# Optimization experiments

Hardware: AMD Instinct MI355X
Metric: run time of the kernel (lower is better)

## Reference

```python
import jax, jax.numpy as jnp
import numpy as np

# NCHW 3x3 conv, padding=1. BatchNorm (inference affine) is folded into conv weight/bias,
# which is mathematically identical to Conv->BN(eval) in the original.
def conv3(x, w, b, stride):
    y = jax.lax.conv_general_dilated(x, w, (stride, stride), [(1, 1), (1, 1)],
                                     dimension_numbers=('NCHW', 'OIHW', 'NCHW'))
    return y + b[None, :, None, None]

def lin1(x, w, b):  # 1x1 conv as channel matmul; w: [out, in]
    return jnp.einsum('oc,bchw->bohw', w, x) + b[None, :, None, None]

def setup_inputs():
    key = jax.random.key(0)
    ks = list(jax.random.split(key, 32))
    C, M = 32, 32  # cv_hypo_num, mid_dim (kq_dim == mid_dim since mid_dim <= 128)
    B, H, W = 1, 256, 512
    w3 = lambda k, o, i: jax.random.normal(k, (o, i, 3, 3), jnp.float32) * 0.05
    w1 = lambda k, o, i: jax.random.normal(k, (o, i), jnp.float32) * 0.05
    bv = lambda k, o: jax.random.normal(k, (o,), jnp.float32) * 0.01
    inp = {
        'mono_pseudo_cost': jax.random.normal(ks[0], (B, C, H, W), jnp.float32),
        'cost_volume': jax.random.normal(ks[1], (B, C, H, W), jnp.float32),
        # mono_expand / multi_expand: two stride-2 conv(+folded BN)+ReLU blocks each
        'me_w1': w3(ks[2], M, C), 'me_b1': bv(ks[3], M),
        'me_w2': w3(ks[4], M, C), 'me_b2': bv(ks[5], M),
        'xe_w1': w3(ks[6], M, C), 'xe_b1': bv(ks[7], M),
        'xe_w2': w3(ks[8], M, C), 'xe_b2': bv(ks[9], M),
        # 1x1 q/k/v projections for both branches
        'mq_w': w1(ks[10], M, M), 'mq_b': bv(ks[11], M),
        'mk_w': w1(ks[12], M, M), 'mk_b': bv(ks[13], M),
        'mv_w': w1(ks[14], M, M), 'mv_b': bv(ks[15], M),
        'xq_w': w1(ks[16], M, M), 'xq_b': bv(ks[17], M),
        'xk_w': w1(ks[18], M, M), 'xk_b': bv(ks[19], M),
        'xv_w': w1(ks[20], M, M), 'xv_b': bv(ks[21], M),
        # residual branches
        'mr_w1': w3(ks[22], M, C), 'mr_b1': bv(ks[23], M),
        'mr_w2': w3(ks[24], M, C), 'mr_b2': bv(ks[25], M),
        'xr_w': w1(ks[26], M, C), 'xr_b': bv(ks[27], M),
        'gamma': jnp.full((1,), 0.5, jnp.float32),  # nonzero so attention path is live
    }
    return inp

def reference(mono_pseudo_cost, cost_volume,
              me_w1, me_b1, me_w2, me_b2,
              xe_w1, xe_b1, xe_w2, xe_b2,
              mq_w, mq_b, mk_w, mk_b, mv_w, mv_b,
              xq_w, xq_b, xk_w, xk_b, xv_w, xv_b,
              mr_w1, mr_b1, mr_w2, mr_b2,
              xr_w, xr_b, gamma):
    relu = jax.nn.relu
    init_h, init_w = cost_volume.shape[2], cost_volume.shape[3]
    M = me_w1.shape[0]
    # feature extractors (stride-2 x2): [B,32,256,512] -> [B,32,64,128]
    mono_feat = relu(conv3(relu(conv3(mono_pseudo_cost, me_w1, me_b1, 2)), me_w2, me_b2, 2))
    multi_feat = relu(conv3(relu(conv3(cost_volume, xe_w1, xe_b1, 2)), xe_w2, xe_b2, 2))
    b, c, h, w = multi_feat.shape
    hw = h * w
    # q/k/v as [B, C, hw]
    mono_q = lin1(mono_feat, mq_w, mq_b).reshape(b, -1, hw)
    mono_k = lin1(mono_feat, mk_w, mk_b).reshape(b, -1, hw)
    mono_v = lin1(mono_feat, mv_w, mv_b).reshape(b, -1, hw)
    multi_q = lin1(multi_feat, xq_w, xq_b).reshape(b, -1, hw)
    multi_k = lin1(multi_feat, xk_w, xk_b).reshape(b, -1, hw)
    multi_v = lin1(multi_feat, xv_w, xv_b).reshape(b, -1, hw)
    # full [B, hw, hw] attention, no 1/sqrt(d) scaling (as in original)
    mono_atten = jax.nn.softmax(jnp.einsum('bci,bcj->bij', mono_q, mono_k), axis=-1)
    multi_atten = jax.nn.softmax(jnp.einsum('bci,bcj->bij', multi_q, multi_k), axis=-1)
    # cross application: mono values weighted by multi attention and vice versa
    mono_out = jnp.einsum('bcj,bij->bci', mono_v, multi_atten).reshape(b, M, h, w)
    multi_out = jnp.einsum('bcj,bij->bci', multi_v, mono_atten).reshape(b, M, h, w)
    fused = jnp.concatenate([multi_out, mono_out], axis=1)
    # nearest-neighbor upsample back to input size (integer factor 4)
    fused = jnp.repeat(jnp.repeat(fused, init_h // h, axis=2), init_w // w, axis=3)
    # residual branches
    mono_residual = relu(conv3(relu(conv3(mono_pseudo_cost, mr_w1, mr_b1, 1)), mr_w2, mr_b2, 1))
    multi_residual = relu(lin1(cost_volume, xr_w, xr_b))
    fused = jnp.concatenate([mono_residual, multi_residual], axis=1) + gamma * fused
    return fused
```

## Files before the change

### kernel.cpp

```cpp
#include <hip/hip_runtime.h>


using bf16x8 = __attribute__((ext_vector_type(8))) short;
using f32x4  = __attribute__((ext_vector_type(4))) float;
using f32x16 = __attribute__((ext_vector_type(16))) float;
typedef unsigned short u16;
typedef unsigned int   u32;

__device__ __forceinline__ u16 f2bf(float f) {
  u32 u = __builtin_bit_cast(u32, f);
  u = (u + 0x7fffu + ((u >> 16) & 1u)) >> 16;
  return (u16)u;
}
__device__ __forceinline__ float bf2f(u16 v) {
  u32 u = ((u32)v) << 16;
  return __builtin_bit_cast(float, u);
}
__device__ __forceinline__ float bfLO(u32 u) { return __builtin_bit_cast(float, u << 16); }
__device__ __forceinline__ float bfHI(u32 u) { return __builtin_bit_cast(float, u & 0xffff0000u); }
__device__ __forceinline__ u32 pktr(float lo, float hi) {
  return __builtin_amdgcn_perm(__builtin_bit_cast(u32, hi),
                               __builtin_bit_cast(u32, lo), 0x07060302u);
}
__device__ __forceinline__ f32x4 mfma16(bf16x8 a, bf16x8 b, f32x4 c) {
  return __builtin_amdgcn_mfma_f32_16x16x32_bf16(a, b, c, 0, 0, 0);
}
__device__ __forceinline__ f32x16 mfma32(bf16x8 a, bf16x8 b, f32x16 c) {
  return __builtin_amdgcn_mfma_f32_32x32x16_bf16(a, b, c, 0, 0, 0);
}
__device__ __forceinline__ f32x16 zero16() {
  f32x16 z = {0,0,0,0,0,0,0,0,0,0,0,0,0,0,0,0};
  return z;
}
__device__ __forceinline__ void store4bf(u16* dst, f32x4 v) {
  u32 lo = (u32)f2bf(v[0]) | ((u32)f2bf(v[1]) << 16);
  u32 hi = (u32)f2bf(v[2]) | ((u32)f2bf(v[3]) << 16);
  *(uint2*)dst = make_uint2(lo, hi);
}
__device__ __forceinline__ float sum16(const float* e) {
  float s0 = e[0] + e[1], s1 = e[2] + e[3], s2 = e[4] + e[5], s3 = e[6] + e[7];
  float s4 = e[8] + e[9], s5 = e[10] + e[11], s6 = e[12] + e[13], s7 = e[14] + e[15];
  float a = s0 + s1, b = s2 + s3, c = s4 + s5, d = s6 + s7;
  return (a + b) + (c + d);
}

struct WPtrs { const float* p[13]; };

__global__ void k_pre(WPtrs wp, u16* __restrict__ wConv, u16* __restrict__ w1x1,
                      const float* __restrict__ mono, const float* __restrict__ cv,
                      u16* __restrict__ monoT, u16* __restrict__ cvT,
                      u16* __restrict__ m1T, u16* __restrict__ x1T, u16* __restrict__ r1T) {
  int bx = blockIdx.x, t = threadIdx.x;
  if (bx < 13) {
    if (bx < 6) {
      const float* s = wp.p[bx];
      u16* d = wConv + bx * 9216;
      for (int i = t; i < 9216; i += 256) {
        int tap = i >> 10, co = (i >> 5) & 31, ci = i & 31;
        d[i] = f2bf(s[co * 288 + ci * 9 + tap]);
      }
    } else {
      const float* s = wp.p[bx];
      u16* d = w1x1 + (bx - 6) * 1024;
      for (int i = t; i < 1024; i += 256) d[i] = f2bf(s[i]);
    }
    return;
  }
  if (bx < 138) {
    int zb = bx - 13;
    int buf = zb % 5, blk = zb / 5;
    u16* b; int Hp, Wp;
    switch (buf) {
      case 0: b = monoT; Hp = 258; Wp = 514; break;
      case 1: b = cvT;   Hp = 258; Wp = 514; break;
      case 2: b = m1T;   Hp = 130; Wp = 258; break;
      case 3: b = x1T;   Hp = 130; Wp = 258; break;
      default: b = r1T;  Hp = 258; Wp = 514; break;
    }
    int id = blk * 256 + t;
    int cell = id >> 2, c8 = (id & 3) << 3;
    if (cell >= 2 * (Hp + Wp)) return;
    int r, c;
    if (cell < Wp)              { r = 0;                 c = cell; }
    else if (cell < 2 * Wp)     { r = Hp - 1;            c = cell - Wp; }
    else if (cell < 2 * Wp + Hp){ r = cell - 2 * Wp;     c = 0; }
    else                        { r = cell - 2 * Wp - Hp; c = Wp - 1; }
    bf16x8 z = {0, 0, 0, 0, 0, 0, 0, 0};
    *(bf16x8*)&b[(r * Wp + c) * 32 + c8] = z;
    return;
  }
  int idx = bx - 138;
  int xb = idx & 7, y = (idx >> 3) & 255, z = idx >> 11;
  const float* src = z ? cv : mono;
  u16* dst = z ? cvT : monoT;
  int x0 = xb << 6;
  __shared__ u16 tile[64][40];
  int ci = t >> 3, kx = (t & 7) << 3;
  const float* sp = src + ci * 131072 + y * 512 + x0 + kx;
  float4 a = *(const float4*)sp;
  float4 bb = *(const float4*)(sp + 4);
  tile[kx + 0][ci] = f2bf(a.x); tile[kx + 1][ci] = f2bf(a.y);
  tile[kx + 2][ci] = f2bf(a.z); tile[kx + 3][ci] = f2bf(a.w);
  tile[kx + 4][ci] = f2bf(bb.x); tile[kx + 5][ci] = f2bf(bb.y);
  tile[kx + 6][ci] = f2bf(bb.z); tile[kx + 7][ci] = f2bf(bb.w);
  __syncthreads();
  int x = t >> 2, c8 = (t & 3) << 3;
  bf16x8 v = *(bf16x8*)&tile[x][c8];
  *(bf16x8*)(dst + ((y + 1) * 514 + (x0 + x + 1)) * 32 + c8) = v;
}

__device__ __forceinline__ void conv3x3_body(int bxl, int tid,
    const u16* __restrict__ inT, int Wp, const u16* __restrict__ w9,
    const float* __restrict__ bias, u16* __restrict__ out, int outPitch,
    int outOff, int Ho, int tprShift, int stride) {
  int wid = (bxl * 256 + tid) >> 6;
  int lane = tid & 63, ln = lane & 15, q = lane >> 4;
  int y = wid >> tprShift;
  int x0 = (wid & ((1 << tprShift) - 1)) << 4;
  if (y >= Ho) return;
  f32x4 acc0 = *(const f32x4*)(bias + q * 4);
  f32x4 acc1 = *(const f32x4*)(bias + 16 + q * 4);
  const u16* ib = inT + (stride * y * Wp + stride * (x0 + ln)) * 32 + q * 8;
  const u16* wb = w9 + ln * 32 + q * 8;
#pragma unroll
  for (int dy = 0; dy < 3; ++dy)
#pragma unroll
    for (int dx = 0; dx < 3; ++dx) {
      int tap = dy * 3 + dx;
      bf16x8 bf = *(const bf16x8*)(ib + (dy * Wp + dx) * 32);
      acc0 = mfma16(*(const bf16x8*)(wb + tap * 1024), bf, acc0);
      acc1 = mfma16(*(const bf16x8*)(wb + tap * 1024 + 512), bf, acc1);
    }
#pragma unroll
  for (int r = 0; r < 4; ++r) { acc0[r] = fmaxf(acc0[r], 0.f); acc1[r] = fmaxf(acc1[r], 0.f); }
  u16* ob = out + (outOff + y * outPitch + x0 + ln) * 32;
  store4bf(ob + q * 4, acc0);
  store4bf(ob + 16 + q * 4, acc1);
}

__global__ void k_convs(const u16* __restrict__ monoT, const u16* __restrict__ cvT,
                        const u16* __restrict__ wConv,
                        const float* me_b1, const float* xe_b1, const float* mr_b1,
                        u16* __restrict__ m1T, u16* __restrict__ x1T, u16* __restrict__ r1T) {
  int bx = blockIdx.x;
  if (bx < 512)
    conv3x3_body(bx, threadIdx.x, monoT, 514, wConv + 0 * 9216, me_b1, m1T, 258, 259, 128, 4, 2);
  else if (bx < 1024)
    conv3x3_body(bx - 512, threadIdx.x, cvT, 514, wConv + 2 * 9216, xe_b1, x1T, 258, 259, 128, 4, 2);
  else
    conv3x3_body(bx - 1024, threadIdx.x, monoT, 514, wConv + 4 * 9216, mr_b1, r1T, 514, 515, 256, 5, 1);
}

__global__ void k_featproj(const u16* __restrict__ m1T, const u16* __restrict__ x1T,
                           const u16* __restrict__ wConv, const u16* __restrict__ w1x1,
                           const float* me_b2, const float* xe_b2,
                           const float* mq_b, const float* mk_b, const float* mv_b,
                           const float* xq_b, const float* xk_b, const float* xv_b,
                           u16* Qm, u16* Km, u16* Vm, u16* Qx, u16* Kx, u16* Vx) {
  int bx = blockIdx.x, br = blockIdx.y;
  const u16* inT = br ? x1T : m1T;
  const u16* w9 = wConv + (br ? 3 : 1) * 9216;
  const float* bias2 = br ? xe_b2 : me_b2;
  __shared__ u16 fs[64][40];
  int tid = threadIdx.x, wave = tid >> 6, lane = tid & 63, ln = lane & 15, q = lane >> 4;
  int fy = bx >> 1, x0 = (bx & 1) * 64 + wave * 16;
  {
    f32x4 acc0 = *(const f32x4*)(bias2 + q * 4);
    f32x4 acc1 = *(const f32x4*)(bias2 + 16 + q * 4);
    const u16* ib = inT + (2 * fy * 258 + 2 * (x0 + ln)) * 32 + q * 8;
    const u16* wb = w9 + ln * 32 + q * 8;
#pragma unroll
    for (int dy = 0; dy < 3; ++dy)
#pragma unroll
      for (int dx = 0; dx < 3; ++dx) {
        int tap = dy * 3 + dx;
        bf16x8 bf = *(const bf16x8*)(ib + (dy * 258 + dx) * 32);
        acc0 = mfma16(*(const bf16x8*)(wb + tap * 1024), bf, acc0);
        acc1 = mfma16(*(const bf16x8*)(wb + tap * 1024 + 512), bf, acc1);
      }
#pragma unroll
    for (int r = 0; r < 4; ++r) { acc0[r] = fmaxf(acc0[r], 0.f); acc1[r] = fmaxf(acc1[r], 0.f); }
    int row = wave * 16 + ln;
    store4bf(&fs[row][q * 4], acc0);
    store4bf(&fs[row][16 + q * 4], acc1);
  }
  __syncthreads();
  int p = fy * 128 + x0 + ln;
  bf16x8 bf = *(const bf16x8*)&fs[wave * 16 + ln][q * 8];
#pragma unroll
  for (int wh = 0; wh < 3; ++wh) {
    int which = br * 3 + wh;
    const float* bias; u16* dst; float scale = 1.f; int cmode = 0;
    switch (which) {
      case 0: bias = mq_b; dst = Qm; scale = 1.4426950408889634f; break;
      case 1: bias = mk_b; dst = Km; break;
      case 2: bias = mv_b; dst = Vm; cmode = 1; break;
      case 3: bias = xq_b; dst = Qx; scale = 1.4426950408889634f; break;
      case 4: bias = xk_b; dst = Kx; break;
      default: bias = xv_b; dst = Vx; cmode = 1; break;
    }
    const u16* w = w1x1 + which * 1024;
    bf16x8 a0 = *(const bf16x8*)(w + ln * 32 + q * 8);
    bf16x8 a1 = *(const bf16x8*)(w + (16 + ln) * 32 + q * 8);
    f32x4 acc0 = *(const f32x4*)(bias + q * 4);
    f32x4 acc1 = *(const f32x4*)(bias + 16 + q * 4);
    acc0 = mfma16(a0, bf, acc0);
    acc1 = mfma16(a1, bf, acc1);
#pragma unroll
    for (int r = 0; r < 4; ++r) { acc0[r] *= scale; acc1[r] *= scale; }
    if (!cmode) {
      store4bf(dst + p * 32 + q * 4, acc0);
      store4bf(dst + p * 32 + 16 + q * 4, acc1);
    } else {
      int jl = p & 63, jb = p & ~63;
      int pj = jb + (jl >> 5) * 32 + ((jl >> 4) & 1) * 16 + ((jl >> 2) & 1) * 8
             + ((jl >> 3) & 1) * 4 + (jl & 3);
#pragma unroll
      for (int r = 0; r < 4; ++r) {
        dst[(q * 4 + r) * 8192 + pj] = f2bf(acc0[r]);
        dst[(16 + q * 4 + r) * 8192 + pj] = f2bf(acc1[r]);
      }
    }
  }
}

__global__ void __launch_bounds__(256, 4) k_attention(
    const u16* __restrict__ Qm, const u16* __restrict__ Km, const u16* __restrict__ Vm,
    const u16* __restrict__ Qx, const u16* __restrict__ Kx, const u16* __restrict__ Vx,
    u16* __restrict__ Opart, float* __restrict__ lpart) {
  const u16 *Qp, *Kp, *Vp;
  int att = blockIdx.z;
  if (att == 0) { Qp = Qm; Kp = Km; Vp = Vx; }
  else          { Qp = Qx; Kp = Kx; Vp = Vm; }
  int sp = blockIdx.y;
  int j0 = sp << 10;

  __shared__ u16 Kl[2][64][40];
  __shared__ u16 Vl[2][32][72];

  int t = threadIdx.x, wave = t >> 6, lane = t & 63, ln = lane & 31, h = lane >> 5;
  int iw = blockIdx.x * 128 + wave * 32;

  bf16x8 qf0 = *(const bf16x8*)(Qp + (iw + ln) * 32 + h * 8);
  bf16x8 qf1 = *(const bf16x8*)(Qp + (iw + ln) * 32 + 16 + h * 8);

  int krow = t >> 2, kcol = (t & 3) << 3;
  int vrow = t >> 3, vcol = (t & 7) << 3;
  const u16* Kg = Kp + j0 * 32;
  const u16* Vg = Vp + j0;

  bf16x8 kn = *(const bf16x8*)(Kg + t * 8);
  bf16x8 vn = *(const bf16x8*)(Vg + vrow * 8192 + vcol);
  *(bf16x8*)&Kl[0][krow][kcol] = kn;
  *(bf16x8*)&Vl[0][vrow][vcol] = vn;

  f32x16 O = zero16();
  float lsum = 0.f;

  for (int jt = 0; jt < 16; ++jt) {
    __syncthreads();
    bool have = (jt + 1) < 16;
    if (have) {
      kn = *(const bf16x8*)(Kg + (jt + 1) * 2048 + t * 8);
      vn = *(const bf16x8*)(Vg + vrow * 8192 + (jt + 1) * 64 + vcol);
    }
    int cur = jt & 1;
#pragma unroll
    for (int hh = 0; hh < 2; ++hh) {
      f32x16 s = mfma32(*(const bf16x8*)&Kl[cur][hh * 32 + ln][h * 8], qf0, zero16());
      s = mfma32(*(const bf16x8*)&Kl[cur][hh * 32 + ln][16 + h * 8], qf1, s);
      float e[16];
#pragma unroll
      for (int r = 0; r < 16; ++r) e[r] = __builtin_amdgcn_exp2f(s[r]);
      lsum += sum16(e);
      union PF { bf16x8 v; u32 w[4]; } pf0, pf1;
#pragma unroll
      for (int p = 0; p < 4; ++p) {
        pf0.w[p] = pktr(e[2 * p], e[2 * p + 1]);
        pf1.w[p] = pktr(e[8 + 2 * p], e[8 + 2 * p + 1]);
      }
      bf16x8 vf0 = *(const bf16x8*)&Vl[cur][ln][(2 * hh) * 16 + h * 8];
      bf16x8 vf1 = *(const bf16x8*)&Vl[cur][ln][(2 * hh + 1) * 16 + h * 8];
      O = mfma32(pf0.v, vf0, O);
      O = mfma32(pf1.v, vf1, O);
    }
    if (have) {
      *(bf16x8*)&Kl[1 - cur][krow][kcol] = kn;
      *(bf16x8*)&Vl[1 - cur][vrow][vcol] = vn;
    }
  }
  u16* ob = Opart + (size_t)(att * 8 + sp) * 262144;
  float* lb = lpart + (att * 8 + sp) * 8192;
#pragma unroll
  for (int r = 0; r < 16; ++r) {
    int ig = iw + (r & 3) + 8 * (r >> 2) + 4 * h;
    ob[ig * 32 + ln] = f2bf(O[r]);
  }
  float lo = __shfl(lsum, lane ^ 32, 64);
  float lt = lsum + lo;
  if (lane < 32) lb[iw + lane] = lt;
}

__device__ __forceinline__ void att_reduce(const u16* __restrict__ Opart,
                                           const float* __restrict__ lpart,
                                           int a, int apix, int q, float g,
                                           f32x4& vA, f32x4& vB) {
  f32x4 sA = {0, 0, 0, 0}, sB = {0, 0, 0, 0};
  float l = 0.f;
#pragma unroll
  for (int sp = 0; sp < 8; ++sp) {
    const u16* op = Opart + (size_t)(a * 8 + sp) * 262144 + apix * 32;
    uint2 w0 = *(const uint2*)(op + q * 4);
    uint2 w1 = *(const uint2*)(op + 16 + q * 4);
    sA[0] += bfLO(w0.x); sA[1] += bfHI(w0.x); sA[2] += bfLO(w0.y); sA[3] += bfHI(w0.y);
    sB[0] += bfLO(w1.x); sB[1] += bfHI(w1.x); sB[2] += bfLO(w1.y); sB[3] += bfHI(w1.y);
    l += lpart[(a * 8 + sp) * 8192 + apix];
  }
  float gl = g / l;
#pragma unroll
  for (int r = 0; r < 4; ++r) { vA[r] = sA[r] * gl; vB[r] = sB[r] * gl; }
}

__global__ void k_final(const u16* __restrict__ r1T, const u16* __restrict__ cvT,
                        const u16* __restrict__ wConv, const u16* __restrict__ w1x1,
                        const float* mr_b2, const float* xr_b,
                        const u16* __restrict__ Opart, const float* __restrict__ lpart,
                        const float* __restrict__ gamma, float* __restrict__ dout) {
  int bx = blockIdx.x, tid = threadIdx.x;
  int lane = tid & 63, ln = lane & 15, q = lane >> 4;
  float g = gamma[0];
  if (bx < 2048) {
    const u16* w9 = wConv + 5 * 9216;
    int wid = (bx * 256 + tid) >> 6;
    int y = wid >> 5, x0 = (wid & 31) << 4;
    f32x4 acc0 = *(const f32x4*)(mr_b2 + q * 4);
    f32x4 acc1 = *(const f32x4*)(mr_b2 + 16 + q * 4);
    const u16* ib = r1T + (y * 514 + x0 + ln) * 32 + q * 8;
    const u16* wb = w9 + ln * 32 + q * 8;
#pragma unroll
    for (int dy = 0; dy < 3; ++dy)
#pragma unroll
      for (int dx = 0; dx < 3; ++dx) {
        int tap = dy * 3 + dx;
        bf16x8 bf = *(const bf16x8*)(ib + (dy * 514 + dx) * 32);
        acc0 = mfma16(*(const bf16x8*)(wb + tap * 1024), bf, acc0);
        acc1 = mfma16(*(const bf16x8*)(wb + tap * 1024 + 512), bf, acc1);
      }
    int xg = x0 + ln;
    int apix = (y >> 2) * 128 + (xg >> 2);
    f32x4 vA, vB;
    att_reduce(Opart, lpart, 0, apix, q, g, vA, vB);
    float* ob = dout + y * 512 + xg;
#pragma unroll
    for (int r = 0; r < 4; ++r) {
      int co0 = q * 4 + r, co1 = 16 + q * 4 + r;
      ob[co0 * 131072] = fmaxf(acc0[r], 0.f) + vA[r];
      ob[co1 * 131072] = fmaxf(acc1[r], 0.f) + vB[r];
    }
  } else {
    const u16* w = w1x1 + 6 * 1024;
    int wid = ((bx - 2048) * 256 + tid) >> 6;
    int p0 = wid << 4;
    int y = p0 >> 9, x0 = p0 & 511;
    bf16x8 bf = *(const bf16x8*)(cvT + ((y + 1) * 514 + x0 + ln + 1) * 32 + q * 8);
    f32x4 acc0 = *(const f32x4*)(xr_b + q * 4);
    f32x4 acc1 = *(const f32x4*)(xr_b + 16 + q * 4);
    acc0 = mfma16(*(const bf16x8*)(w + ln * 32 + q * 8), bf, acc0);
    acc1 = mfma16(*(const bf16x8*)(w + (16 + ln) * 32 + q * 8), bf, acc1);
    int xg = x0 + ln;
    int apix = (y >> 2) * 128 + (xg >> 2);
    f32x4 vA, vB;
    att_reduce(Opart, lpart, 1, apix, q, g, vA, vB);
    float* ob = dout + 32 * 131072 + p0 + ln;
#pragma unroll
    for (int r = 0; r < 4; ++r) {
      int co0 = q * 4 + r, co1 = 16 + q * 4 + r;
      ob[co0 * 131072] = fmaxf(acc0[r], 0.f) + vA[r];
      ob[co1 * 131072] = fmaxf(acc1[r], 0.f) + vB[r];
    }
  }
}

extern "C" void kernel_launch(void* const* d_in, const int* in_sizes, int n_in,
                              void* d_out, int out_size, void* d_ws, size_t ws_size,
                              hipStream_t stream) {
  const float* mono  = (const float*)d_in[0];
  const float* cv    = (const float*)d_in[1];
  const float* me_b1 = (const float*)d_in[3];
  const float* me_b2 = (const float*)d_in[5];
  const float* xe_b1 = (const float*)d_in[7];
  const float* xe_b2 = (const float*)d_in[9];
  const float* mq_b  = (const float*)d_in[11];
  const float* mk_b  = (const float*)d_in[13];
  const float* mv_b  = (const float*)d_in[15];
  const float* xq_b  = (const float*)d_in[17];
  const float* xk_b  = (const float*)d_in[19];
  const float* xv_b  = (const float*)d_in[21];
  const float* mr_b1 = (const float*)d_in[23];
  const float* mr_b2 = (const float*)d_in[25];
  const float* xr_b  = (const float*)d_in[27];
  const float* gamma = (const float*)d_in[28];
  float* dout = (float*)d_out;

  char* ws = (char*)d_ws;
  u16* wConv = (u16*)(ws + 0);
  u16* w1x1  = (u16*)(ws + 110592);
  u16* monoT = (u16*)(ws + 124928);
  u16* Opart = (u16*)(ws + 124928);
  u16* cvT   = (u16*)(ws + 8612096);
  u16* m1T   = (u16*)(ws + 17099264);
  u16* x1T   = (u16*)(ws + 19245824);
  u16* r1T   = (u16*)(ws + 21392384);
  u16* Qm    = (u16*)(ws + 30928128);
  u16* Km    = (u16*)(ws + 31452416);
  u16* Vm    = (u16*)(ws + 31976704);
  u16* Qx    = (u16*)(ws + 32500992);
  u16* Kx    = (u16*)(ws + 33025280);
  u16* Vx    = (u16*)(ws + 33549568);
  float* lpart = (float*)(ws + 36171008);

  WPtrs wp;
  wp.p[0] = (const float*)d_in[2];
  wp.p[1] = (const float*)d_in[4];
  wp.p[2] = (const float*)d_in[6];
  wp.p[3] = (const float*)d_in[8];
  wp.p[4] = (const float*)d_in[22];
  wp.p[5] = (const float*)d_in[24];
  wp.p[6] = (const float*)d_in[10];
  wp.p[7] = (const float*)d_in[12];
  wp.p[8] = (const float*)d_in[14];
  wp.p[9] = (const float*)d_in[16];
  wp.p[10] = (const float*)d_in[18];
  wp.p[11] = (const float*)d_in[20];
  wp.p[12] = (const float*)d_in[26];

  k_pre<<<4234, 256, 0, stream>>>(wp, wConv, w1x1, mono, cv, monoT, cvT, m1T, x1T, r1T);
  k_convs<<<3072, 256, 0, stream>>>(monoT, cvT, wConv, me_b1, xe_b1, mr_b1, m1T, x1T, r1T);
  k_featproj<<<dim3(128, 2), 256, 0, stream>>>(m1T, x1T, wConv, w1x1, me_b2, xe_b2,
                                               mq_b, mk_b, mv_b, xq_b, xk_b, xv_b,
                                               Qm, Km, Vm, Qx, Kx, Vx);
  k_attention<<<dim3(64, 8, 2), 256, 0, stream>>>(Qm, Km, Vm, Qx, Kx, Vx, Opart, lpart);
  k_final<<<4096, 256, 0, stream>>>(r1T, cvT, wConv, w1x1, mr_b2, xr_b, Opart, lpart, gamma, dout);
}
```

Before: 214.6 us.

## Fuse residual full-res conv into attention launch and double attention K/V tile

```diff
diff --git a/kernel.cpp b/kernel.cpp
--- a/kernel.cpp
+++ b/kernel.cpp
@@ -140,15 +140,13 @@
 
 __global__ void k_convs(const u16* __restrict__ monoT, const u16* __restrict__ cvT,
                         const u16* __restrict__ wConv,
-                        const float* me_b1, const float* xe_b1, const float* mr_b1,
-                        u16* __restrict__ m1T, u16* __restrict__ x1T, u16* __restrict__ r1T) {
+                        const float* me_b1, const float* xe_b1,
+                        u16* __restrict__ m1T, u16* __restrict__ x1T) {
   int bx = blockIdx.x;
   if (bx < 512)
     conv3x3_body(bx, threadIdx.x, monoT, 514, wConv + 0 * 9216, me_b1, m1T, 258, 259, 128, 4, 2);
-  else if (bx < 1024)
+  else
     conv3x3_body(bx - 512, threadIdx.x, cvT, 514, wConv + 2 * 9216, xe_b1, x1T, 258, 259, 128, 4, 2);
-  else
-    conv3x3_body(bx - 1024, threadIdx.x, monoT, 514, wConv + 4 * 9216, mr_b1, r1T, 514, 515, 256, 5, 1);
 }
 
 __global__ void k_featproj(const u16* __restrict__ m1T, const u16* __restrict__ x1T,
@@ -224,51 +222,62 @@
   }
 }
 
-__global__ void __launch_bounds__(256, 4) k_attention(
+__global__ void __launch_bounds__(256, 4) k_attnconv(
     const u16* __restrict__ Qm, const u16* __restrict__ Km, const u16* __restrict__ Vm,
     const u16* __restrict__ Qx, const u16* __restrict__ Kx, const u16* __restrict__ Vx,
-    u16* __restrict__ Opart, float* __restrict__ lpart) {
+    const u16* __restrict__ monoT, const u16* __restrict__ wConv, const float* mr_b1,
+    u16* __restrict__ r1T, u16* __restrict__ Opart, float* __restrict__ lpart) {
+  int vb = blockIdx.x;
+  if (vb >= 1024) {
+    conv3x3_body(vb - 1024, threadIdx.x, monoT, 514, wConv + 4 * 9216, mr_b1,
+                 r1T, 514, 515, 256, 5, 1);
+    return;
+  }
+  int ib = vb & 63, sp = (vb >> 6) & 7, att = vb >> 9;
   const u16 *Qp, *Kp, *Vp;
-  int att = blockIdx.z;
   if (att == 0) { Qp = Qm; Kp = Km; Vp = Vx; }
   else          { Qp = Qx; Kp = Kx; Vp = Vm; }
-  int sp = blockIdx.y;
-  int j0 = sp << 10;
-
-  __shared__ u16 Kl[2][64][40];
-  __shared__ u16 Vl[2][32][72];
+
+  __shared__ u16 Kl[2][128][40];
+  __shared__ u16 Vl[2][32][136];
 
   int t = threadIdx.x, wave = t >> 6, lane = t & 63, ln = lane & 31, h = lane >> 5;
-  int iw = blockIdx.x * 128 + wave * 32;
+  int iw = ib * 128 + wave * 32;
 
   bf16x8 qf0 = *(const bf16x8*)(Qp + (iw + ln) * 32 + h * 8);
   bf16x8 qf1 = *(const bf16x8*)(Qp + (iw + ln) * 32 + 16 + h * 8);
 
-  int krow = t >> 2, kcol = (t & 3) << 3;
-  int vrow = t >> 3, vcol = (t & 7) << 3;
-  const u16* Kg = Kp + j0 * 32;
-  const u16* Vg = Vp + j0;
-
-  bf16x8 kn = *(const bf16x8*)(Kg + t * 8);
-  bf16x8 vn = *(const bf16x8*)(Vg + vrow * 8192 + vcol);
-  *(bf16x8*)&Kl[0][krow][kcol] = kn;
-  *(bf16x8*)&Vl[0][vrow][vcol] = vn;
+  int krow = t >> 1, kcol = (t & 1) << 4;
+  int vrow = t >> 3, vcol = (t & 7) << 4;
+  const u16* Kg = Kp + sp * 32768;
+  const u16* Vg = Vp + sp * 1024;
+
+  bf16x8 kn0 = *(const bf16x8*)(Kg + t * 16);
+  bf16x8 kn1 = *(const bf16x8*)(Kg + t * 16 + 8);
+  bf16x8 vn0 = *(const bf16x8*)(Vg + vrow * 8192 + vcol);
+  bf16x8 vn1 = *(const bf16x8*)(Vg + vrow * 8192 + vcol + 8);
+  *(bf16x8*)&Kl[0][krow][kcol] = kn0;
+  *(bf16x8*)&Kl[0][krow][kcol + 8] = kn1;
+  *(bf16x8*)&Vl[0][vrow][vcol] = vn0;
+  *(bf16x8*)&Vl[0][vrow][vcol + 8] = vn1;
 
   f32x16 O = zero16();
   float lsum = 0.f;
 
-  for (int jt = 0; jt < 16; ++jt) {
+  for (int jt = 0; jt < 8; ++jt) {
     __syncthreads();
-    bool have = (jt + 1) < 16;
+    bool have = (jt + 1) < 8;
     if (have) {
-      kn = *(const bf16x8*)(Kg + (jt + 1) * 2048 + t * 8);
-      vn = *(const bf16x8*)(Vg + vrow * 8192 + (jt + 1) * 64 + vcol);
+      kn0 = *(const bf16x8*)(Kg + (jt + 1) * 4096 + t * 16);
+      kn1 = *(const bf16x8*)(Kg + (jt + 1) * 4096 + t * 16 + 8);
+      vn0 = *(const bf16x8*)(Vg + vrow * 8192 + (jt + 1) * 128 + vcol);
+      vn1 = *(const bf16x8*)(Vg + vrow * 8192 + (jt + 1) * 128 + vcol + 8);
     }
     int cur = jt & 1;
 #pragma unroll
-    for (int hh = 0; hh < 2; ++hh) {
-      f32x16 s = mfma32(*(const bf16x8*)&Kl[cur][hh * 32 + ln][h * 8], qf0, zero16());
-      s = mfma32(*(const bf16x8*)&Kl[cur][hh * 32 + ln][16 + h * 8], qf1, s);
+    for (int g = 0; g < 4; ++g) {
+      f32x16 s = mfma32(*(const bf16x8*)&Kl[cur][g * 32 + ln][h * 8], qf0, zero16());
+      s = mfma32(*(const bf16x8*)&Kl[cur][g * 32 + ln][16 + h * 8], qf1, s);
       float e[16];
 #pragma unroll
       for (int r = 0; r < 16; ++r) e[r] = __builtin_amdgcn_exp2f(s[r]);
@@ -279,14 +288,16 @@
         pf0.w[p] = pktr(e[2 * p], e[2 * p + 1]);
         pf1.w[p] = pktr(e[8 + 2 * p], e[8 + 2 * p + 1]);
       }
-      bf16x8 vf0 = *(const bf16x8*)&Vl[cur][ln][(2 * hh) * 16 + h * 8];
-      bf16x8 vf1 = *(const bf16x8*)&Vl[cur][ln][(2 * hh + 1) * 16 + h * 8];
+      bf16x8 vf0 = *(const bf16x8*)&Vl[cur][ln][g * 32 + h * 8];
+      bf16x8 vf1 = *(const bf16x8*)&Vl[cur][ln][g * 32 + 16 + h * 8];
       O = mfma32(pf0.v, vf0, O);
       O = mfma32(pf1.v, vf1, O);
     }
     if (have) {
-      *(bf16x8*)&Kl[1 - cur][krow][kcol] = kn;
-      *(bf16x8*)&Vl[1 - cur][vrow][vcol] = vn;
+      *(bf16x8*)&Kl[1 - cur][krow][kcol] = kn0;
+      *(bf16x8*)&Kl[1 - cur][krow][kcol + 8] = kn1;
+      *(bf16x8*)&Vl[1 - cur][vrow][vcol] = vn0;
+      *(bf16x8*)&Vl[1 - cur][vrow][vcol + 8] = vn1;
     }
   }
   u16* ob = Opart + (size_t)(att * 8 + sp) * 262144;
@@ -406,7 +417,6 @@
   u16* wConv = (u16*)(ws + 0);
   u16* w1x1  = (u16*)(ws + 110592);
   u16* monoT = (u16*)(ws + 124928);
-  u16* Opart = (u16*)(ws + 124928);
   u16* cvT   = (u16*)(ws + 8612096);
   u16* m1T   = (u16*)(ws + 17099264);
   u16* x1T   = (u16*)(ws + 19245824);
@@ -418,6 +428,7 @@
   u16* Kx    = (u16*)(ws + 33025280);
   u16* Vx    = (u16*)(ws + 33549568);
   float* lpart = (float*)(ws + 36171008);
+  u16* Opart = (u16*)(ws + 37219840);
 
   WPtrs wp;
   wp.p[0] = (const float*)d_in[2];
@@ -435,10 +446,11 @@
   wp.p[12] = (const float*)d_in[26];
 
   k_pre<<<4234, 256, 0, stream>>>(wp, wConv, w1x1, mono, cv, monoT, cvT, m1T, x1T, r1T);
-  k_convs<<<3072, 256, 0, stream>>>(monoT, cvT, wConv, me_b1, xe_b1, mr_b1, m1T, x1T, r1T);
+  k_convs<<<1024, 256, 0, stream>>>(monoT, cvT, wConv, me_b1, xe_b1, m1T, x1T);
   k_featproj<<<dim3(128, 2), 256, 0, stream>>>(m1T, x1T, wConv, w1x1, me_b2, xe_b2,
                                                mq_b, mk_b, mv_b, xq_b, xk_b, xv_b,
                                                Qm, Km, Vm, Qx, Kx, Vx);
-  k_attention<<<dim3(64, 8, 2), 256, 0, stream>>>(Qm, Km, Vm, Qx, Kx, Vx, Opart, lpart);
+  k_attnconv<<<3072, 256, 0, stream>>>(Qm, Km, Vm, Qx, Kx, Vx,
+                                       monoT, wConv, mr_b1, r1T, Opart, lpart);
   k_final<<<4096, 256, 0, stream>>>(r1T, cvT, wConv, w1x1, mr_b2, xr_b, Opart, lpart, gamma, dout);
 }
```

Result: no change. 210.7 us (-1.8%).
